# Kernel tuning notes

Measured on AMD Instinct MI355X. Metric: run time of the kernel, lower is better.

## Reference

```python
import jax, jax.numpy as jnp
import numpy as np

D_MODEL = 512
D_STATE = 128
D_CONV = 4
D_INNER = 1024
HEADDIM = 64
NHEADS = 16
CONV_DIM = D_INNER + 2 * D_STATE          # 1280
D_IN_PROJ = 2 * D_INNER + 2 * D_STATE + NHEADS  # 2320
N_LAYER = 28
VOCAB = 256
EPS = 1e-5
BATCH = 16
SEQ = 768


def _rms(x, w):
    return x * jax.lax.rsqrt(jnp.mean(x * x, axis=-1, keepdims=True) + EPS) * w


def _ssd(x, dt, A, Bm, Cm):
    # x [B,L,H,P], dt [B,L,H], A [H], Bm/Cm [B,L,N] (ngroups=1, broadcast over heads)
    Bb, L, H, P = x.shape
    N = Bm.shape[-1]
    dA = jnp.exp(dt * A)          # [B,L,H] discrete decay
    dBx = dt[..., None] * x       # [B,L,H,P]

    def step(h, t):
        dA_t, dBx_t, B_t, C_t = t
        # h: [B,H,P,N]
        h = dA_t[:, :, None, None] * h + dBx_t[..., None] * B_t[:, None, None, :]
        y = jnp.einsum('bhpn,bn->bhp', h, C_t)
        return h, y

    h0 = jnp.zeros((Bb, H, P, N), x.dtype)
    xs = (jnp.moveaxis(dA, 1, 0), jnp.moveaxis(dBx, 1, 0),
          jnp.moveaxis(Bm, 1, 0), jnp.moveaxis(Cm, 1, 0))
    _, ys = jax.lax.scan(step, h0, xs)
    return jnp.moveaxis(ys, 0, 1)  # [B,L,H,P]


def _mamba2(u, p):
    # u: [B,L,D_MODEL]
    Bb, L, _ = u.shape
    zxbcdt = u @ p['in_proj_w'].T                      # [B,L,2320]
    z = zxbcdt[..., :D_INNER]
    xBC = zxbcdt[..., D_INNER:D_INNER + CONV_DIM]
    dt = jax.nn.softplus(zxbcdt[..., D_INNER + CONV_DIM:] + p['dt_bias'])  # [B,L,H]
    # causal depthwise conv1d (kernel 4) + silu
    xp = jnp.pad(xBC, ((0, 0), (D_CONV - 1, 0), (0, 0)))
    conv = sum(xp[:, k:k + L, :] * p['conv_w'][:, k] for k in range(D_CONV)) + p['conv_b']
    xBC = jax.nn.silu(conv)
    x = xBC[..., :D_INNER].reshape(Bb, L, NHEADS, HEADDIM)
    Bm = xBC[..., D_INNER:D_INNER + D_STATE]
    Cm = xBC[..., D_INNER + D_STATE:]
    A = -jnp.exp(p['A_log'])                           # [H]
    y = _ssd(x, dt, A, Bm, Cm) + p['D'][None, None, :, None] * x
    y = y.reshape(Bb, L, D_INNER)
    # RMSNormGated (norm_before_gate=False): norm(y * silu(z)) * w
    y = _rms(y * jax.nn.silu(z), p['gnorm_w'])
    return y @ p['out_proj_w'].T


def _forward(tokens, targets, params):
    hidden = params['embedding'][tokens]               # [B,L,D]
    residual = jnp.zeros_like(hidden)

    layer_params = {k: params[k] for k in
                    ('in_proj_w', 'conv_w', 'conv_b', 'dt_bias', 'A_log',
                     'D', 'gnorm_w', 'out_proj_w', 'block_norm_w')}

    def layer(carry, lp):
        h, res = carry
        res = h + res
        h = _rms(res, lp['block_norm_w'])
        h = _mamba2(h, lp)
        return (h, res), None

    (hidden, residual), _ = jax.lax.scan(layer, (hidden, residual), layer_params)
    hidden = _rms(hidden + residual, params['norm_f_w'])
    logits = hidden @ params['embedding'].T            # tied lm_head
    logp = jax.nn.log_softmax(logits, axis=-1)
    loss = -jnp.mean(jnp.take_along_axis(logp, targets[..., None], axis=-1))
    return logits, loss


def setup_inputs():
    key = jax.random.key(0)
    ks = jax.random.split(key, 12)
    tokens = jax.random.randint(ks[0], (BATCH, SEQ), 0, VOCAB, dtype=jnp.int32)
    targets = jax.random.randint(ks[1], (BATCH, SEQ), 0, VOCAB, dtype=jnp.int32)
    embedding = jax.random.normal(ks[2], (VOCAB, D_MODEL), jnp.float32) * 0.02
    in_proj_w = jax.random.normal(ks[3], (N_LAYER, D_IN_PROJ, D_MODEL), jnp.float32) * (D_MODEL ** -0.5)
    conv_w = jax.random.normal(ks[4], (N_LAYER, CONV_DIM, D_CONV), jnp.float32) * 0.2
    conv_b = jnp.zeros((N_LAYER, CONV_DIM), jnp.float32)
    dt0 = jnp.exp(jax.random.uniform(ks[5], (N_LAYER, NHEADS)) * (np.log(0.1) - np.log(1e-3)) + np.log(1e-3))
    dt_bias = dt0 + jnp.log(-jnp.expm1(-dt0))          # inverse softplus
    A_log = jnp.log(jax.random.uniform(ks[6], (N_LAYER, NHEADS), minval=1.0, maxval=16.0))
    Dp = jnp.ones((N_LAYER, NHEADS), jnp.float32)
    gnorm_w = jnp.ones((N_LAYER, D_INNER), jnp.float32)
    out_proj_w = jax.random.normal(ks[7], (N_LAYER, D_MODEL, D_INNER), jnp.float32) * (D_INNER ** -0.5 / np.sqrt(N_LAYER))
    block_norm_w = jnp.ones((N_LAYER, D_MODEL), jnp.float32)
    norm_f_w = jnp.ones((D_MODEL,), jnp.float32)
    return {'tokens': tokens, 'targets': targets, 'embedding': embedding,
            'in_proj_w': in_proj_w, 'conv_w': conv_w, 'conv_b': conv_b,
            'dt_bias': dt_bias, 'A_log': A_log, 'D': Dp, 'gnorm_w': gnorm_w,
            'out_proj_w': out_proj_w, 'block_norm_w': block_norm_w, 'norm_f_w': norm_f_w}


def reference(tokens, targets, embedding, in_proj_w, conv_w, conv_b, dt_bias,
              A_log, D, gnorm_w, out_proj_w, block_norm_w, norm_f_w):
    params = {'embedding': embedding, 'in_proj_w': in_proj_w, 'conv_w': conv_w,
              'conv_b': conv_b, 'dt_bias': dt_bias, 'A_log': A_log, 'D': D,
              'gnorm_w': gnorm_w, 'out_proj_w': out_proj_w,
              'block_norm_w': block_norm_w, 'norm_f_w': norm_f_w}
    return _forward(tokens, targets, params)
```

## Files before the change

kernel.cpp:

```cpp
#include <hip/hip_runtime.h>
#include <hip/hip_bf16.h>
#include <math.h>

#define BATCH   16
#define SEQ     768
#define DMODEL  512
#define DSTATE  128
#define DINNER  1024
#define NHEADS  16
#define HEADDIM 64
#define CONVDIM 1280
#define DINPROJ 2320
#define DINPROJP 2432
#define DTBASE  2304
#define NLAYER  28
#define VOCABSZ 256
#define NROWS   (BATCH*SEQ)
#define EPSV    1e-5f
#define NCH     8
#define CH      96
#define STATESZ (HEADDIM*DSTATE)

typedef __hip_bfloat16 bf16_t;
typedef __attribute__((ext_vector_type(8))) __bf16 bf16x8;
typedef __attribute__((ext_vector_type(4))) float floatx4;

__device__ __forceinline__ float siluf(float v) { return v / (1.f + expf(-v)); }

__device__ __forceinline__ void gload_lds16(const bf16_t* g, bf16_t* l) {
  __builtin_amdgcn_global_load_lds(
      (const __attribute__((address_space(1))) unsigned int*)g,
      (__attribute__((address_space(3))) unsigned int*)l, 16, 0, 0);
}

__global__ __launch_bounds__(256) void embed_kernel(const int* __restrict__ tok,
    const float* __restrict__ emb, float* __restrict__ hid, float* __restrict__ res,
    bf16_t* __restrict__ w_emb_bf) {
  int i = blockIdx.x * 256 + threadIdx.x;
  const int total = NROWS * DMODEL;
  if (i < total) {
    int r = i >> 9;
    int d = i & (DMODEL - 1);
    hid[i] = emb[(size_t)tok[r] * DMODEL + d];
    res[i] = 0.f;
  } else {
    int j = i - total;
    if (j < VOCABSZ * DMODEL) w_emb_bf[j] = __float2bfloat16(emb[j]);
  }
}

__global__ __launch_bounds__(256) void cvt_weights_kernel(const float* __restrict__ ipw,
    const float* __restrict__ opw, bf16_t* __restrict__ win, bf16_t* __restrict__ wout) {
  int i = blockIdx.x * 256 + threadIdx.x;
  const int n1 = DINPROJP * DMODEL;
  if (i < n1) {
    int row = i >> 9, col = i & (DMODEL - 1);
    float v = (row < DINPROJ) ? ipw[(size_t)row * DMODEL + col] : 0.f;
    win[i] = __float2bfloat16(v);
  } else {
    int j = i - n1;
    if (j < DMODEL * DINNER) wout[j] = __float2bfloat16(opw[j]);
  }
}

__global__ __launch_bounds__(128) void prenorm_kernel(const float* __restrict__ h,
    float* __restrict__ res, const float* __restrict__ w, bf16_t* __restrict__ xn) {
  int row = blockIdx.x;
  int tid = threadIdx.x;
  const float4* h4 = (const float4*)(h + (size_t)row * DMODEL);
  float4* r4 = (float4*)(res + (size_t)row * DMODEL);
  float4 v = r4[tid];
  float4 a = h4[tid];
  v.x += a.x; v.y += a.y; v.z += a.z; v.w += a.w;
  r4[tid] = v;
  float ss = v.x * v.x + v.y * v.y + v.z * v.z + v.w * v.w;
  #pragma unroll
  for (int o = 32; o > 0; o >>= 1) ss += __shfl_down(ss, o);
  __shared__ float wred[2];
  if ((tid & 63) == 0) wred[tid >> 6] = ss;
  __syncthreads();
  float tot = wred[0] + wred[1];
  float scale = rsqrtf(tot / (float)DMODEL + EPSV);
  const float4* w4 = (const float4*)w;
  float4 wv = w4[tid];
  union { bf16_t b[4]; uint2 u; } pk;
  pk.b[0] = __float2bfloat16(v.x * scale * wv.x);
  pk.b[1] = __float2bfloat16(v.y * scale * wv.y);
  pk.b[2] = __float2bfloat16(v.z * scale * wv.z);
  pk.b[3] = __float2bfloat16(v.w * scale * wv.w);
  ((uint2*)(xn + (size_t)row * DMODEL))[tid] = pk.u;
}

template<int BN, typename TO>
__global__ __launch_bounds__(256) void gemm_bf16_bt(const bf16_t* __restrict__ A,
    const bf16_t* __restrict__ B, TO* __restrict__ C, float* __restrict__ aux,
    int M, int N, int K) {
  constexpr int JF = BN / 32;
  __shared__ bf16_t As[128 * 32];
  __shared__ bf16_t Bs[BN * 32];
  int tid = threadIdx.x;
  int m0 = blockIdx.y * 128;
  int n0 = blockIdx.x * BN;
  int w = tid >> 6, lane = tid & 63;
  int wm = (w >> 1) * 64, wn = (w & 1) * (BN / 2);
  int l16 = lane & 15, lq = lane >> 4;
  floatx4 acc[4][JF];
  #pragma unroll
  for (int i = 0; i < 4; ++i)
    #pragma unroll
    for (int j = 0; j < JF; ++j)
      acc[i][j] = (floatx4){0.f, 0.f, 0.f, 0.f};
  int arow0 = tid >> 2, ak0 = (tid & 3) * 8;
  const bf16_t* Abase = A + (size_t)m0 * K;
  const bf16_t* Bbase = B + (size_t)n0 * K;
  bf16_t* AsW = As + (w << 9);
  bf16_t* BsW = Bs + (w << 9);
  for (int k0 = 0; k0 < K; k0 += 32) {
    __syncthreads();
    gload_lds16(Abase + (size_t)arow0 * K + k0 + ak0, AsW);
    gload_lds16(Abase + (size_t)(arow0 + 64) * K + k0 + ak0, AsW + 2048);
    gload_lds16(Bbase + (size_t)arow0 * K + k0 + ak0, BsW);
    if (BN == 128)
      gload_lds16(Bbase + (size_t)(arow0 + 64) * K + k0 + ak0, BsW + 2048);
    __syncthreads();
    bf16x8 af[4], bfr[JF];
    #pragma unroll
    for (int i = 0; i < 4; ++i)
      af[i] = *(const bf16x8*)(As + (wm + i * 16 + l16) * 32 + lq * 8);
    #pragma unroll
    for (int j = 0; j < JF; ++j)
      bfr[j] = *(const bf16x8*)(Bs + (wn + j * 16 + l16) * 32 + lq * 8);
    #pragma unroll
    for (int i = 0; i < 4; ++i)
      #pragma unroll
      for (int j = 0; j < JF; ++j)
        acc[i][j] = __builtin_amdgcn_mfma_f32_16x16x32_bf16(af[i], bfr[j], acc[i][j], 0, 0, 0);
  }
  #pragma unroll
  for (int i = 0; i < 4; ++i) {
    #pragma unroll
    for (int j = 0; j < JF; ++j) {
      int n = n0 + wn + j * 16 + l16;
      if (n < N) {
        int mb = m0 + wm + i * 16 + lq * 4;
        #pragma unroll
        for (int r = 0; r < 4; ++r) {
          float vv = acc[i][j][r];
          if constexpr (sizeof(TO) == 2)
            C[(size_t)(mb + r) * N + n] = __float2bfloat16(vv);
          else
            C[(size_t)(mb + r) * N + n] = vv;
          if (aux && n >= DTBASE)
            aux[(size_t)(mb + r) * NHEADS + (n - DTBASE)] = vv;
        }
      }
    }
  }
}

__global__ __launch_bounds__(320) void convdt_kernel(const bf16_t* __restrict__ zx,
    const float* __restrict__ dtcol, const float* __restrict__ cw,
    const float* __restrict__ cb, const float* __restrict__ dt_bias,
    const float* __restrict__ A_log, bf16_t* __restrict__ out,
    float* __restrict__ dt, float* __restrict__ ldA) {
  int bl0 = blockIdx.x * 4;
  int t0 = bl0 % SEQ;
  int tid = threadIdx.x;
  int c = tid * 4;
  const bf16_t* base = zx + (size_t)bl0 * DINPROJ + DINNER + c;
  float4 v[7];
  #pragma unroll
  for (int k = 0; k < 7; ++k) {
    int tt = t0 + k - 3;
    if (tt >= 0) {
      union { ushort4 u; bf16_t b[4]; } q;
      q.u = *(const ushort4*)(base + (ptrdiff_t)(k - 3) * DINPROJ);
      v[k] = make_float4(__bfloat162float(q.b[0]), __bfloat162float(q.b[1]),
                         __bfloat162float(q.b[2]), __bfloat162float(q.b[3]));
    } else {
      v[k] = make_float4(0.f, 0.f, 0.f, 0.f);
    }
  }
  float4 w0 = *(const float4*)(cw + (size_t)(c + 0) * 4);
  float4 w1 = *(const float4*)(cw + (size_t)(c + 1) * 4);
  float4 w2 = *(const float4*)(cw + (size_t)(c + 2) * 4);
  float4 w3 = *(const float4*)(cw + (size_t)(c + 3) * 4);
  float4 bias = *(const float4*)(cb + c);
  const float* w0f = (const float*)&w0;
  const float* w1f = (const float*)&w1;
  const float* w2f = (const float*)&w2;
  const float* w3f = (const float*)&w3;
  #pragma unroll
  for (int j = 0; j < 4; ++j) {
    float4 acc = bias;
    #pragma unroll
    for (int k = 0; k < 4; ++k) {
      float4 vv = v[j + k];
      acc.x += vv.x * w0f[k];
      acc.y += vv.y * w1f[k];
      acc.z += vv.z * w2f[k];
      acc.w += vv.w * w3f[k];
    }
    union { ushort4 u; bf16_t b[4]; } pk;
    pk.b[0] = __float2bfloat16(siluf(acc.x));
    pk.b[1] = __float2bfloat16(siluf(acc.y));
    pk.b[2] = __float2bfloat16(siluf(acc.z));
    pk.b[3] = __float2bfloat16(siluf(acc.w));
    *(ushort4*)(out + (size_t)(bl0 + j) * CONVDIM + c) = pk.u;
  }
  if (tid < 64) {
    int j = tid >> 4, h = tid & 15;
    int bl = bl0 + j;
    float vv = dtcol[(size_t)bl * NHEADS + h] + dt_bias[h];
    float sp = fmaxf(vv, 0.f) + log1pf(expf(-fabsf(vv)));
    float Ah = -expf(A_log[h]);
    dt[bl * NHEADS + h] = sp;
    ldA[bl * NHEADS + h] = sp * Ah;
  }
}

__global__ __launch_bounds__(512) void scan_mfma_kernel(const bf16_t* __restrict__ conv,
    const float* __restrict__ dtb, const float* __restrict__ ldAb,
    const float* __restrict__ Dp, float* __restrict__ y,
    float* __restrict__ state, float* __restrict__ chunkprod) {
  const int c  = blockIdx.x;
  const int b  = blockIdx.y >> 1;
  const int h0 = (blockIdx.y & 1) * 8;
  const int tid  = threadIdx.x;
  const int w    = tid >> 6;
  const int lane = tid & 63;
  const size_t row0 = (size_t)(b * SEQ + c * CH);

  __shared__ __align__(16) bf16_t Bb[96 * 136];
  __shared__ __align__(16) bf16_t Cb[96 * 136];
  __shared__ __align__(16) bf16_t Pl[96 * 104];
  __shared__ __align__(16) bf16_t xT[64 * 104];
  __shared__ __align__(16) bf16_t BTw[128 * 104];
  __shared__ float ldas[8][96];
  __shared__ float dts[8][96];
  __shared__ float cums[8][96];
  __shared__ float wts[8][96];

  for (int i = tid; i < 96 * 32; i += 512) {
    int t = i >> 5, g = i & 31;
    bf16x8 v = *(const bf16x8*)(conv + (row0 + t) * CONVDIM + DINNER + g * 8);
    if (g < 16) *(bf16x8*)(Bb + t * 136 + g * 8) = v;
    else        *(bf16x8*)(Cb + t * 136 + (g - 16) * 8) = v;
  }
  for (int i = tid; i < 768; i += 512) {
    int hh = i & 7, t = i >> 3;
    size_t gi = (row0 + t) * NHEADS + h0 + hh;
    dts[hh][t]  = dtb[gi];
    ldas[hh][t] = ldAb[gi];
  }
  __syncthreads();
  if (tid < 8) {
    float cacc = 0.f;
    for (int t = 0; t < 96; ++t) { cacc += ldas[tid][t]; cums[tid][t] = cacc; }
  }
  __syncthreads();
  for (int i = tid; i < 768; i += 512) {
    int hh = i & 7, t = i >> 3;
    wts[hh][t] = expf(cums[hh][95] - cums[hh][t]) * dts[hh][t];
  }
  if (tid < 8)
    chunkprod[(b * NHEADS + h0 + tid) * NCH + c] = expf(cums[tid][95]);

  floatx4 gacc[5];
  #pragma unroll
  for (int it = 0; it < 5; ++it) gacc[it] = (floatx4){0.f, 0.f, 0.f, 0.f};
  const int l16 = lane & 15, lk = (lane >> 4) << 3;
  #pragma unroll
  for (int it = 0; it < 5; ++it) {
    int tt = w + it * 8;
    int ti = (tt < 36) ? (tt / 6) : 0;
    int si = (tt < 36) ? (tt % 6) : 0;
    #pragma unroll
    for (int ks = 0; ks < 4; ++ks) {
      bf16x8 a = *(const bf16x8*)(Cb + (ti * 16 + l16) * 136 + ks * 32 + lk);
      bf16x8 bb = *(const bf16x8*)(Bb + (si * 16 + l16) * 136 + ks * 32 + lk);
      gacc[it] = __builtin_amdgcn_mfma_f32_16x16x32_bf16(a, bb, gacc[it], 0, 0, 0);
    }
  }

  for (int hh = 0; hh < 8; ++hh) {
    __syncthreads();
    for (int i = tid; i < 768; i += 512) {
      int t = i >> 3, p8 = (i & 7) * 8;
      union { bf16x8 v8; unsigned short s[8]; } u;
      u.v8 = *(const bf16x8*)(conv + (row0 + t) * CONVDIM + (h0 + hh) * HEADDIM + p8);
      #pragma unroll
      for (int r = 0; r < 8; ++r)
        ((unsigned short*)xT)[(p8 + r) * 104 + t] = u.s[r];
    }
    for (int i = tid; i < 128 * 96; i += 512) {
      int n = i / 96, t = i - n * 96;
      float bv = __bfloat162float(Bb[t * 136 + n]);
      BTw[n * 104 + t] = __float2bfloat16(wts[hh][t] * bv);
    }
    #pragma unroll
    for (int it = 0; it < 5; ++it) {
      int tt = w + it * 8;
      if (tt < 36) {
        int ti = tt / 6, si = tt % 6;
        int scol = si * 16 + l16;
        #pragma unroll
        for (int r = 0; r < 4; ++r) {
          int trow = ti * 16 + ((lane >> 4) << 2) + r;
          float pv = 0.f;
          if (scol <= trow)
            pv = expf(cums[hh][trow] - cums[hh][scol]) * dts[hh][scol] * gacc[it][r];
          Pl[trow * 104 + scol] = __float2bfloat16(pv);
        }
      }
    }
    __syncthreads();
    float Dh = Dp[h0 + hh];
    #pragma unroll
    for (int it = 0; it < 3; ++it) {
      int tt = w + it * 8;
      int ti = tt >> 2, pi = tt & 3;
      floatx4 acc = (floatx4){0.f, 0.f, 0.f, 0.f};
      #pragma unroll
      for (int ks = 0; ks < 3; ++ks) {
        bf16x8 a = *(const bf16x8*)(Pl + (ti * 16 + l16) * 104 + ks * 32 + lk);
        bf16x8 bb = *(const bf16x8*)(xT + (pi * 16 + l16) * 104 + ks * 32 + lk);
        acc = __builtin_amdgcn_mfma_f32_16x16x32_bf16(a, bb, acc, 0, 0, 0);
      }
      int p = pi * 16 + l16;
      #pragma unroll
      for (int r = 0; r < 4; ++r) {
        int t = ti * 16 + ((lane >> 4) << 2) + r;
        float xg = __bfloat162float(conv[(row0 + t) * CONVDIM + (h0 + hh) * HEADDIM + p]);
        y[((row0 + t) * NHEADS + h0 + hh) * HEADDIM + p] = acc[r] + Dh * xg;
      }
    }
    size_t sb = ((size_t)(b * NHEADS + h0 + hh) * NCH + c) * STATESZ;
    #pragma unroll
    for (int it = 0; it < 4; ++it) {
      int tt = w + it * 8;
      int ni = tt >> 2, pi = tt & 3;
      floatx4 acc = (floatx4){0.f, 0.f, 0.f, 0.f};
      #pragma unroll
      for (int ks = 0; ks < 3; ++ks) {
        bf16x8 a = *(const bf16x8*)(BTw + (ni * 16 + l16) * 104 + ks * 32 + lk);
        bf16x8 bb = *(const bf16x8*)(xT + (pi * 16 + l16) * 104 + ks * 32 + lk);
        acc = __builtin_amdgcn_mfma_f32_16x16x32_bf16(a, bb, acc, 0, 0, 0);
      }
      int p = pi * 16 + l16;
      #pragma unroll
      for (int r = 0; r < 4; ++r) {
        int n = ni * 16 + ((lane >> 4) << 2) + r;
        state[sb + (size_t)n * HEADDIM + p] = acc[r];
      }
    }
  }
}

__global__ __launch_bounds__(256) void state_combine_kernel(float* __restrict__ state,
    const float* __restrict__ cprod) {
  int bh = blockIdx.y;
  int sl = blockIdx.x;
  int tid = threadIdx.x;
  float4* slab = (float4*)(state + (size_t)bh * NCH * STATESZ) + sl * 256 + tid;
  const float* pc = cprod + bh * NCH;
  float4 H = make_float4(0.f, 0.f, 0.f, 0.f);
  for (int c = 1; c < NCH; ++c) {
    float P = pc[c - 1];
    float4* sp = slab + (size_t)(c - 1) * (STATESZ / 4);
    float4 S = *sp;
    H.x = P * H.x + S.x; H.y = P * H.y + S.y;
    H.z = P * H.z + S.z; H.w = P * H.w + S.w;
    *sp = H;
  }
}

__global__ __launch_bounds__(256) void ycorr_kernel(const bf16_t* __restrict__ conv,
    const float* __restrict__ ldAb, const float* __restrict__ state,
    float* __restrict__ y) {
  int c = blockIdx.x + 1;
  int bh = blockIdx.y;
  int b = bh >> 4, h = bh & 15;
  int tid = threadIdx.x;
  __shared__ float Cs[CH][DSTATE];
  __shared__ float cA[CH];
  const int tstart = c * CH;

  if (tid < CH) cA[tid] = ldAb[((size_t)(b * SEQ + tstart + tid)) * NHEADS + h];
  __syncthreads();
  for (int off = 1; off < CH; off <<= 1) {
    float tmp = 0.f;
    if (tid < CH && tid >= off) tmp = cA[tid - off];
    __syncthreads();
    if (tid < CH) cA[tid] += tmp;
    __syncthreads();
  }
  if (tid < CH) cA[tid] = expf(cA[tid]);
  __syncthreads();

  const bf16_t* Cg = conv + (size_t)(b * SEQ + tstart) * CONVDIM + DINNER + DSTATE;
  #pragma unroll
  for (int j = 0; j < 6; ++j) {
    int idx = j * 256 + tid;
    int row = idx >> 4, col8 = (idx & 15) * 8;
    bf16x8 v = *(const bf16x8*)(Cg + (size_t)row * CONVDIM + col8);
    float a = cA[row];
    float4 lo, hi;
    lo.x = a * (float)v[0]; lo.y = a * (float)v[1];
    lo.z = a * (float)v[2]; lo.w = a * (float)v[3];
    hi.x = a * (float)v[4]; hi.y = a * (float)v[5];
    hi.z = a * (float)v[6]; hi.w = a * (float)v[7];
    *(float4*)&Cs[row][col8] = lo;
    *(float4*)&Cs[row][col8 + 4] = hi;
  }
  __syncthreads();

  int s = tid >> 6, p = tid & 63;
  const float* Hb = state + ((size_t)bh * NCH + (c - 1)) * STATESZ + p;
  float acc[CH / 4];
  #pragma unroll
  for (int i = 0; i < CH / 4; ++i) acc[i] = 0.f;
  for (int n = 0; n < DSTATE; n += 4) {
    float h0 = Hb[(size_t)(n + 0) * HEADDIM];
    float h1 = Hb[(size_t)(n + 1) * HEADDIM];
    float h2 = Hb[(size_t)(n + 2) * HEADDIM];
    float h3 = Hb[(size_t)(n + 3) * HEADDIM];
    #pragma unroll
    for (int i = 0; i < CH / 4; ++i) {
      int tt = s + i * 4;
      float4 Cv = *(const float4*)&Cs[tt][n];
      acc[i] += Cv.x * h0 + Cv.y * h1 + Cv.z * h2 + Cv.w * h3;
    }
  }
  #pragma unroll
  for (int i = 0; i < CH / 4; ++i) {
    int tt = s + i * 4;
    size_t yi = ((size_t)(b * SEQ + tstart + tt) * NHEADS + h) * HEADDIM + p;
    y[yi] += acc[i];
  }
}

__global__ __launch_bounds__(256) void gated_norm_kernel(const float* __restrict__ y,
    const bf16_t* __restrict__ zx, const float* __restrict__ gw, bf16_t* __restrict__ out) {
  int row = blockIdx.x;
  int tid = threadIdx.x;
  const float4* y4 = (const float4*)(y + (size_t)row * DINNER);
  float4 yv = y4[tid];
  union { ushort4 u; bf16_t b[4]; } zq;
  zq.u = ((const ushort4*)(zx + (size_t)row * DINPROJ))[tid];
  float4 zv = make_float4(__bfloat162float(zq.b[0]), __bfloat162float(zq.b[1]),
                          __bfloat162float(zq.b[2]), __bfloat162float(zq.b[3]));
  float4 g;
  g.x = yv.x * siluf(zv.x); g.y = yv.y * siluf(zv.y);
  g.z = yv.z * siluf(zv.z); g.w = yv.w * siluf(zv.w);
  float ss = g.x * g.x + g.y * g.y + g.z * g.z + g.w * g.w;
  #pragma unroll
  for (int o = 32; o > 0; o >>= 1) ss += __shfl_down(ss, o);
  __shared__ float red[4];
  if ((tid & 63) == 0) red[tid >> 6] = ss;
  __syncthreads();
  float tot = red[0] + red[1] + red[2] + red[3];
  float scale = rsqrtf(tot / (float)DINNER + EPSV);
  const float4* g4 = (const float4*)gw;
  float4 wv = g4[tid];
  union { bf16_t b[4]; uint2 u; } pk;
  pk.b[0] = __float2bfloat16(g.x * scale * wv.x);
  pk.b[1] = __float2bfloat16(g.y * scale * wv.y);
  pk.b[2] = __float2bfloat16(g.z * scale * wv.z);
  pk.b[3] = __float2bfloat16(g.w * scale * wv.w);
  ((uint2*)(out + (size_t)row * DINNER))[tid] = pk.u;
}

__global__ __launch_bounds__(256) void rowloss_kernel(const float* __restrict__ logits,
    const int* __restrict__ targets, float* __restrict__ rl) {
  int row = blockIdx.x * 4 + (threadIdx.x >> 6);
  int lane = threadIdx.x & 63;
  const float* lr = logits + (size_t)row * VOCABSZ;
  float4 v = ((const float4*)lr)[lane];
  float mx = fmaxf(fmaxf(v.x, v.y), fmaxf(v.z, v.w));
  #pragma unroll
  for (int o = 32; o > 0; o >>= 1) mx = fmaxf(mx, __shfl_down(mx, o));
  mx = __shfl(mx, 0);
  float e = expf(v.x - mx) + expf(v.y - mx) + expf(v.z - mx) + expf(v.w - mx);
  #pragma unroll
  for (int o = 32; o > 0; o >>= 1) e += __shfl_down(e, o);
  if (lane == 0) {
    float lse = logf(e) + mx;
    rl[row] = lse - lr[targets[row]];
  }
}

__global__ __launch_bounds__(256) void loss_reduce_kernel(const float* __restrict__ rl,
    float* __restrict__ out) {
  int tid = threadIdx.x;
  float ssum = 0.f;
  for (int i = tid; i < NROWS; i += 256) ssum += rl[i];
  #pragma unroll
  for (int o = 32; o > 0; o >>= 1) ssum += __shfl_down(ssum, o);
  __shared__ float red[4];
  if ((tid & 63) == 0) red[tid >> 6] = ssum;
  __syncthreads();
  if (tid == 0) out[0] = (red[0] + red[1] + red[2] + red[3]) / (float)NROWS;
}

extern "C" void kernel_launch(void* const* d_in, const int* in_sizes, int n_in,
                              void* d_out, int out_size, void* d_ws, size_t ws_size,
                              hipStream_t stream) {
  const int*   tokens       = (const int*)d_in[0];
  const int*   targets      = (const int*)d_in[1];
  const float* embedding    = (const float*)d_in[2];
  const float* in_proj_w    = (const float*)d_in[3];
  const float* conv_w       = (const float*)d_in[4];
  const float* conv_b       = (const float*)d_in[5];
  const float* dt_bias      = (const float*)d_in[6];
  const float* A_log        = (const float*)d_in[7];
  const float* Dp           = (const float*)d_in[8];
  const float* gnorm_w      = (const float*)d_in[9];
  const float* out_proj_w   = (const float*)d_in[10];
  const float* block_norm_w = (const float*)d_in[11];
  const float* norm_f_w     = (const float*)d_in[12];
  float* out = (float*)d_out;

  float* ws = (float*)d_ws;
  size_t off = 0;
  float* hidden   = ws + off; off += (size_t)NROWS * DMODEL;
  float* residual = ws + off; off += (size_t)NROWS * DMODEL;
  bf16_t* zx      = (bf16_t*)(ws + off); off += (size_t)NROWS * DINPROJ / 2;
  float* dtcol    = ws + off; off += (size_t)NROWS * NHEADS;
  bf16_t* convo   = (bf16_t*)(ws + off); off += (size_t)NROWS * CONVDIM / 2;
  float* dtb      = ws + off; off += (size_t)NROWS * NHEADS;
  float* ldAb     = ws + off; off += (size_t)NROWS * NHEADS;
  float* ybuf     = ws + off; off += (size_t)NROWS * DINNER;
  float* cprod    = ws + off; off += (size_t)BATCH * NHEADS * NCH;
  float* rowloss  = ws + off; off += NROWS;
  bf16_t* w_in_bf  = (bf16_t*)(ws + off); off += (size_t)DINPROJP * DMODEL / 2;
  bf16_t* w_out_bf = (bf16_t*)(ws + off); off += (size_t)DMODEL * DINNER / 2;
  bf16_t* w_emb_bf = (bf16_t*)(ws + off); off += (size_t)VOCABSZ * DMODEL / 2;
  float*  state  = ws + off;
  bf16_t* xn_bf  = (bf16_t*)(ws + off);
  bf16_t* yn_bf  = (bf16_t*)(ws + off);
  off += (size_t)BATCH * NHEADS * NCH * STATESZ;

  embed_kernel<<<(NROWS * DMODEL + VOCABSZ * DMODEL) / 256, 256, 0, stream>>>(
      tokens, embedding, hidden, residual, w_emb_bf);

  const int cvt_total = DINPROJP * DMODEL + DMODEL * DINNER;
  for (int l = 0; l < NLAYER; ++l) {
    const float* ipw = in_proj_w + (size_t)l * DINPROJ * DMODEL;
    const float* cw  = conv_w + (size_t)l * CONVDIM * 4;
    const float* cb  = conv_b + (size_t)l * CONVDIM;
    const float* dtbias_l = dt_bias + (size_t)l * NHEADS;
    const float* alog_l   = A_log + (size_t)l * NHEADS;
    const float* D_l      = Dp + (size_t)l * NHEADS;
    const float* gw  = gnorm_w + (size_t)l * DINNER;
    const float* opw = out_proj_w + (size_t)l * DMODEL * DINNER;
    const float* bnw = block_norm_w + (size_t)l * DMODEL;

    cvt_weights_kernel<<<(cvt_total + 255) / 256, 256, 0, stream>>>(ipw, opw, w_in_bf, w_out_bf);
    prenorm_kernel<<<NROWS, 128, 0, stream>>>(hidden, residual, bnw, xn_bf);
    dim3 g1(DINPROJP / 128, NROWS / 128);
    gemm_bf16_bt<128, bf16_t><<<g1, 256, 0, stream>>>(xn_bf, w_in_bf, zx, dtcol,
                                                      NROWS, DINPROJ, DMODEL);
    convdt_kernel<<<NROWS / 4, 320, 0, stream>>>(zx, dtcol, cw, cb, dtbias_l, alog_l,
                                                 convo, dtb, ldAb);
    scan_mfma_kernel<<<dim3(NCH, BATCH * 2), 512, 0, stream>>>(
        convo, dtb, ldAb, D_l, ybuf, state, cprod);
    state_combine_kernel<<<dim3(NCH, BATCH * NHEADS), 256, 0, stream>>>(state, cprod);
    ycorr_kernel<<<dim3(NCH - 1, BATCH * NHEADS), 256, 0, stream>>>(
        convo, ldAb, state, ybuf);
    gated_norm_kernel<<<NROWS, 256, 0, stream>>>(ybuf, zx, gw, yn_bf);
    dim3 g2(DMODEL / 64, NROWS / 128);
    gemm_bf16_bt<64, float><<<g2, 256, 0, stream>>>(yn_bf, w_out_bf, hidden, nullptr,
                                                    NROWS, DMODEL, DINNER);
  }

  prenorm_kernel<<<NROWS, 128, 0, stream>>>(hidden, residual, norm_f_w, xn_bf);
  dim3 g3(VOCABSZ / 64, NROWS / 128);
  gemm_bf16_bt<64, float><<<g3, 256, 0, stream>>>(xn_bf, w_emb_bf, out, nullptr,
                                                  NROWS, VOCABSZ, DMODEL);
  rowloss_kernel<<<NROWS / 4, 256, 0, stream>>>(out, targets, rowloss);
  loss_reduce_kernel<<<1, 256, 0, stream>>>(rowloss, out + (size_t)(out_size - 1));
}
```

Baseline: 9.025 ms.

## Rewrite inter-chunk output correction with bf16 MFMA and reuse scan cumsums

Replaces the scalar FP32 ycorr kernel with an MFMA-based version that computes C·H^T per chunk in bf16 tiles, handling 8 heads per block and sharing the C tile across them. The scan kernel now writes its per-chunk cumulative log-decay to a new buffer, so the correction kernel skips its own prefix sum. Block count drops from 7x256 to 7x32 blocks of 512 threads, which cuts parallelism. The carried state is rounded to bf16 before the matmul, which may reduce accuracy.

```diff
diff --git a/kernel.cpp b/kernel.cpp
--- a/kernel.cpp
+++ b/kernel.cpp
@@ -222,7 +222,8 @@
 __global__ __launch_bounds__(512) void scan_mfma_kernel(const bf16_t* __restrict__ conv,
     const float* __restrict__ dtb, const float* __restrict__ ldAb,
     const float* __restrict__ Dp, float* __restrict__ y,
-    float* __restrict__ state, float* __restrict__ chunkprod) {
+    float* __restrict__ state, float* __restrict__ chunkprod,
+    float* __restrict__ cumb) {
   const int c  = blockIdx.x;
   const int b  = blockIdx.y >> 1;
   const int h0 = (blockIdx.y & 1) * 8;
@@ -262,6 +263,7 @@
   for (int i = tid; i < 768; i += 512) {
     int hh = i & 7, t = i >> 3;
     wts[hh][t] = expf(cums[hh][95] - cums[hh][t]) * dts[hh][t];
+    cumb[(row0 + t) * NHEADS + h0 + hh] = cums[hh][t];
   }
   if (tid < 8)
     chunkprod[(b * NHEADS + h0 + tid) * NCH + c] = expf(cums[tid][95]);
@@ -375,68 +377,59 @@
   }
 }
 
-__global__ __launch_bounds__(256) void ycorr_kernel(const bf16_t* __restrict__ conv,
-    const float* __restrict__ ldAb, const float* __restrict__ state,
+__global__ __launch_bounds__(512) void ycorr_mfma_kernel(const bf16_t* __restrict__ conv,
+    const float* __restrict__ cumb, const float* __restrict__ state,
     float* __restrict__ y) {
-  int c = blockIdx.x + 1;
-  int bh = blockIdx.y;
-  int b = bh >> 4, h = bh & 15;
-  int tid = threadIdx.x;
-  __shared__ float Cs[CH][DSTATE];
-  __shared__ float cA[CH];
-  const int tstart = c * CH;
-
-  if (tid < CH) cA[tid] = ldAb[((size_t)(b * SEQ + tstart + tid)) * NHEADS + h];
-  __syncthreads();
-  for (int off = 1; off < CH; off <<= 1) {
-    float tmp = 0.f;
-    if (tid < CH && tid >= off) tmp = cA[tid - off];
+  const int c  = blockIdx.x + 1;
+  const int b  = blockIdx.y >> 1;
+  const int h0 = (blockIdx.y & 1) * 8;
+  const int tid  = threadIdx.x;
+  const int w    = tid >> 6;
+  const int lane = tid & 63;
+  const int l16 = lane & 15, lk = (lane >> 4) << 3;
+  const size_t row0 = (size_t)(b * SEQ + c * CH);
+
+  __shared__ __align__(16) bf16_t Cb[96 * 136];
+  __shared__ __align__(16) bf16_t HT[64 * 136];
+  __shared__ float cAs[8][96];
+
+  for (int i = tid; i < 96 * 16; i += 512) {
+    int t = i >> 4, g = i & 15;
+    bf16x8 v = *(const bf16x8*)(conv + (row0 + t) * CONVDIM + DINNER + DSTATE + g * 8);
+    *(bf16x8*)(Cb + t * 136 + g * 8) = v;
+  }
+  for (int i = tid; i < 768; i += 512) {
+    int hh = i & 7, t = i >> 3;
+    cAs[hh][t] = expf(cumb[(row0 + t) * NHEADS + h0 + hh]);
+  }
+
+  for (int hh = 0; hh < 8; ++hh) {
     __syncthreads();
-    if (tid < CH) cA[tid] += tmp;
+    const float* Hs = state + ((size_t)(b * NHEADS + h0 + hh) * NCH + (c - 1)) * STATESZ;
+    for (int i = tid; i < STATESZ; i += 512) {
+      int n = i >> 6, p = i & 63;
+      HT[p * 136 + n] = __float2bfloat16(Hs[i]);
+    }
     __syncthreads();
-  }
-  if (tid < CH) cA[tid] = expf(cA[tid]);
-  __syncthreads();
-
-  const bf16_t* Cg = conv + (size_t)(b * SEQ + tstart) * CONVDIM + DINNER + DSTATE;
-  #pragma unroll
-  for (int j = 0; j < 6; ++j) {
-    int idx = j * 256 + tid;
-    int row = idx >> 4, col8 = (idx & 15) * 8;
-    bf16x8 v = *(const bf16x8*)(Cg + (size_t)row * CONVDIM + col8);
-    float a = cA[row];
-    float4 lo, hi;
-    lo.x = a * (float)v[0]; lo.y = a * (float)v[1];
-    lo.z = a * (float)v[2]; lo.w = a * (float)v[3];
-    hi.x = a * (float)v[4]; hi.y = a * (float)v[5];
-    hi.z = a * (float)v[6]; hi.w = a * (float)v[7];
-    *(float4*)&Cs[row][col8] = lo;
-    *(float4*)&Cs[row][col8 + 4] = hi;
-  }
-  __syncthreads();
-
-  int s = tid >> 6, p = tid & 63;
-  const float* Hb = state + ((size_t)bh * NCH + (c - 1)) * STATESZ + p;
-  float acc[CH / 4];
-  #pragma unroll
-  for (int i = 0; i < CH / 4; ++i) acc[i] = 0.f;
-  for (int n = 0; n < DSTATE; n += 4) {
-    float h0 = Hb[(size_t)(n + 0) * HEADDIM];
-    float h1 = Hb[(size_t)(n + 1) * HEADDIM];
-    float h2 = Hb[(size_t)(n + 2) * HEADDIM];
-    float h3 = Hb[(size_t)(n + 3) * HEADDIM];
-    #pragma unroll
-    for (int i = 0; i < CH / 4; ++i) {
-      int tt = s + i * 4;
-      float4 Cv = *(const float4*)&Cs[tt][n];
-      acc[i] += Cv.x * h0 + Cv.y * h1 + Cv.z * h2 + Cv.w * h3;
-    }
-  }
-  #pragma unroll
-  for (int i = 0; i < CH / 4; ++i) {
-    int tt = s + i * 4;
-    size_t yi = ((size_t)(b * SEQ + tstart + tt) * NHEADS + h) * HEADDIM + p;
-    y[yi] += acc[i];
+    #pragma unroll
+    for (int it = 0; it < 3; ++it) {
+      int tt = w + it * 8;
+      int ti = tt >> 2, pi = tt & 3;
+      floatx4 acc = (floatx4){0.f, 0.f, 0.f, 0.f};
+      #pragma unroll
+      for (int ks = 0; ks < 4; ++ks) {
+        bf16x8 a = *(const bf16x8*)(Cb + (ti * 16 + l16) * 136 + ks * 32 + lk);
+        bf16x8 bb = *(const bf16x8*)(HT + (pi * 16 + l16) * 136 + ks * 32 + lk);
+        acc = __builtin_amdgcn_mfma_f32_16x16x32_bf16(a, bb, acc, 0, 0, 0);
+      }
+      int p = pi * 16 + l16;
+      #pragma unroll
+      for (int r = 0; r < 4; ++r) {
+        int t = ti * 16 + ((lane >> 4) << 2) + r;
+        size_t yi = ((row0 + t) * NHEADS + h0 + hh) * HEADDIM + p;
+        y[yi] += cAs[hh][t] * acc[r];
+      }
+    }
   }
 }
 
@@ -530,6 +523,7 @@
   bf16_t* convo   = (bf16_t*)(ws + off); off += (size_t)NROWS * CONVDIM / 2;
   float* dtb      = ws + off; off += (size_t)NROWS * NHEADS;
   float* ldAb     = ws + off; off += (size_t)NROWS * NHEADS;
+  float* cumbuf   = ws + off; off += (size_t)NROWS * NHEADS;
   float* ybuf     = ws + off; off += (size_t)NROWS * DINNER;
   float* cprod    = ws + off; off += (size_t)BATCH * NHEADS * NCH;
   float* rowloss  = ws + off; off += NROWS;
@@ -564,10 +558,10 @@
     convdt_kernel<<<NROWS / 4, 320, 0, stream>>>(zx, dtcol, cw, cb, dtbias_l, alog_l,
                                                  convo, dtb, ldAb);
     scan_mfma_kernel<<<dim3(NCH, BATCH * 2), 512, 0, stream>>>(
-        convo, dtb, ldAb, D_l, ybuf, state, cprod);
+        convo, dtb, ldAb, D_l, ybuf, state, cprod, cumbuf);
     state_combine_kernel<<<dim3(NCH, BATCH * NHEADS), 256, 0, stream>>>(state, cprod);
-    ycorr_kernel<<<dim3(NCH - 1, BATCH * NHEADS), 256, 0, stream>>>(
-        convo, ldAb, state, ybuf);
+    ycorr_mfma_kernel<<<dim3(NCH - 1, BATCH * 2), 512, 0, stream>>>(
+        convo, cumbuf, state, ybuf);
     gated_norm_kernel<<<NROWS, 256, 0, stream>>>(ybuf, zx, gw, yn_bf);
     dim3 g2(DMODEL / 64, NROWS / 128);
     gemm_bf16_bt<64, float><<<g2, 256, 0, stream>>>(yn_bf, w_out_bf, hidden, nullptr,
```

New measurement: 7.587 ms. 1.19x faster.
